# Kernel optimization log

Hardware: AMD Instinct MI355X
Metric: run time of the kernel (lower is better)

## Reference

```python
import jax, jax.numpy as jnp
import numpy as np

HIDDEN = 1024
N_HEADS = 16
HEAD_DIM = HIDDEN // N_HEADS  # 64; RoPE applied only to first HEAD_DIM channels (head 0)
NUM_BUCKETS = 32
MAX_DISTANCE = 128
MLP_HIDDEN = 4 * HIDDEN
B, N = 2, 2048


def _rotate_half(x):
    # interleaved pairs [a0,b0,a1,b1,...] -> [-b0,a0,-b1,a1,...]
    sh = x.shape
    xr = x.reshape(sh[:-1] + (sh[-1] // 2, 2))
    x1, x2 = xr[..., 0], xr[..., 1]
    return jnp.stack([-x2, x1], axis=-1).reshape(sh)


def _rel_bucket(n, num_buckets=NUM_BUCKETS, max_distance=MAX_DISTANCE):
    # bidirectional T5 bucketing
    ctx = jnp.arange(n)[:, None]
    mem = jnp.arange(n)[None, :]
    rp = mem - ctx  # [n, n]
    nb = num_buckets // 2
    buckets = jnp.where(rp > 0, nb, 0)
    rp = jnp.abs(rp)
    max_exact = nb // 2
    is_small = rp < max_exact
    log_ratio = jnp.log(jnp.maximum(rp, 1).astype(jnp.float32) / max_exact)
    rpl = max_exact + (log_ratio / np.log(max_distance / max_exact) * (nb - max_exact)).astype(jnp.int32)
    rpl = jnp.minimum(rpl, nb - 1)
    return buckets + jnp.where(is_small, rp, rpl)


def _ln(x, eps=1e-6):
    # LayerNorm without affine (DiT elementwise_affine=False)
    m = jnp.mean(x, axis=-1, keepdims=True)
    v = jnp.mean(jnp.square(x - m), axis=-1, keepdims=True)
    return (x - m) * jax.lax.rsqrt(v + eps)


def setup_inputs() -> dict:
    key = jax.random.key(0)
    ks = jax.random.split(key, 12)
    s = 0.02
    return {
        "x": jax.random.normal(ks[0], (B, N, HIDDEN), dtype=jnp.float32),
        "c": jax.random.normal(ks[1], (B, HIDDEN), dtype=jnp.float32),
        "w_ada": jax.random.normal(ks[2], (HIDDEN, 6 * HIDDEN), dtype=jnp.float32) * s,
        "b_ada": jnp.zeros((6 * HIDDEN,), dtype=jnp.float32),
        "w_qkv": jax.random.normal(ks[3], (HIDDEN, 3 * HIDDEN), dtype=jnp.float32) * s,
        "b_qkv": jnp.zeros((3 * HIDDEN,), dtype=jnp.float32),
        "w_out": jax.random.normal(ks[4], (HIDDEN, HIDDEN), dtype=jnp.float32) * s,
        "b_out": jnp.zeros((HIDDEN,), dtype=jnp.float32),
        "rel_table": jax.random.normal(ks[5], (NUM_BUCKETS, N_HEADS), dtype=jnp.float32) * s,
        "w_mlp1": jax.random.normal(ks[6], (HIDDEN, MLP_HIDDEN), dtype=jnp.float32) * s,
        "b_mlp1": jnp.zeros((MLP_HIDDEN,), dtype=jnp.float32),
        "w_mlp2": jax.random.normal(ks[7], (MLP_HIDDEN, HIDDEN), dtype=jnp.float32) * s,
        "b_mlp2": jnp.zeros((HIDDEN,), dtype=jnp.float32),
    }


def reference(x, c, w_ada, b_ada, w_qkv, b_qkv, w_out, b_out, rel_table,
              w_mlp1, b_mlp1, w_mlp2, b_mlp2):
    Bb, n, hid = x.shape
    hd = HEAD_DIM

    # AdaLN-Zero modulation params from conditioning
    mod = jax.nn.silu(c) @ w_ada + b_ada  # [B, 6*hid]
    sh_msa, sc_msa, g_msa, sh_mlp, sc_mlp, g_mlp = jnp.split(mod, 6, axis=-1)

    # --- attention branch ---
    h = _ln(x) * (1.0 + sc_msa[:, None, :]) + sh_msa[:, None, :]
    qkv = h @ w_qkv + b_qkv
    q, k, v = jnp.split(qkv, 3, axis=-1)  # each [B, N, hid]

    # partial RoPE: only first head_dim channels (head 0), interleaved-duplicated freqs
    t = jnp.arange(n, dtype=jnp.float32)
    inv_freq = 1.0 / (10000.0 ** (jnp.arange(0, hd, 2, dtype=jnp.float32) / hd))
    fr = t[:, None] * inv_freq[None, :]               # [N, hd/2]
    fr = jnp.stack([fr, fr], axis=-1).reshape(n, hd)  # [N, hd] interleaved dup
    cos, sin = jnp.cos(fr)[None], jnp.sin(fr)[None]

    def partial_rope(a):
        r, u = a[..., :hd], a[..., hd:]
        r = r * cos + _rotate_half(r) * sin
        return jnp.concatenate([r, u], axis=-1)

    q = partial_rope(q)
    k = partial_rope(k)

    qh = q.reshape(Bb, n, N_HEADS, hd)
    kh = k.reshape(Bb, n, N_HEADS, hd)
    vh = v.reshape(Bb, n, N_HEADS, hd)

    scores = jnp.einsum('bqhd,bkhd->bhqk', qh, kh) / np.float32(np.sqrt(hd))
    bias = rel_table[_rel_bucket(n)]                 # [N, N, H]
    scores = scores + jnp.transpose(bias, (2, 0, 1))[None]  # [1,H,N,N]
    attn = jax.nn.softmax(scores, axis=-1)
    ctxv = jnp.einsum('bhqk,bkhd->bqhd', attn, vh).reshape(Bb, n, hid)
    attn_out = ctxv @ w_out + b_out
    x = x + g_msa[:, None, :] * attn_out

    # --- MLP branch ---
    h2 = _ln(x) * (1.0 + sc_mlp[:, None, :]) + sh_mlp[:, None, :]
    m = jax.nn.gelu(h2 @ w_mlp1 + b_mlp1, approximate=True) @ w_mlp2 + b_mlp2
    return x + g_mlp[:, None, :] * m
```

## Files before the change

### kernel.cpp

```cpp
#include <hip/hip_runtime.h>
#include <hip/hip_bf16.h>

#define SEQ 2048

typedef float f32x4 __attribute__((ext_vector_type(4)));
typedef float f32x16 __attribute__((ext_vector_type(16)));
typedef short short8 __attribute__((ext_vector_type(8)));
typedef int int4v __attribute__((ext_vector_type(4)));

static __device__ __forceinline__ unsigned short f2bf(float f) {
  __hip_bfloat16 h = __float2bfloat16(f);
  unsigned short u;
  __builtin_memcpy(&u, &h, 2);
  return u;
}
static __device__ __forceinline__ float bf2f(unsigned short u) {
  __hip_bfloat16 h;
  __builtin_memcpy(&h, &u, 2);
  return __bfloat162float(h);
}
static __device__ __forceinline__ void gload16(const void* g, void* l) {
  __builtin_amdgcn_global_load_lds(
      (const __attribute__((address_space(1))) void*)g,
      (__attribute__((address_space(3))) void*)l, 16, 0, 0);
}
static __device__ __forceinline__ float gelu_t(float x) {
  float t = x * x;
  float z = x * fmaf(0.1029442695044937f, t, 2.3021181827964594f);
  return x * __builtin_amdgcn_rcpf(1.f + exp2f(-z));
}
static __device__ __forceinline__ unsigned int cvtpk(float lo, float hi) {
  unsigned int r;
  asm("v_cvt_pk_bf16_f32 %0, %1, %2" : "=v"(r) : "v"(lo), "v"(hi));
  return r;
}
static __device__ __forceinline__ void rope_pair(short8& v, int m, int i, float pos) {
  const float fr = exp2f(-(float)(2 * i) * (13.287712379549449f / 64.f));
  const float ang = pos * fr;
  const float sn = sinf(ang), cs = cosf(ang);
  const float x0 = bf2f((unsigned short)v[2 * m]);
  const float x1 = bf2f((unsigned short)v[2 * m + 1]);
  v[2 * m] = (short)f2bf(x0 * cs - x1 * sn);
  v[2 * m + 1] = (short)f2bf(x1 * cs + x0 * sn);
}


#define SOFTMAX_M0 16.0f
__global__ void prep_misc(const float* __restrict__ c, float* __restrict__ siluc,
                          const float* __restrict__ rel_table, float* __restrict__ brp) {
  const int bid = blockIdx.x, t = threadIdx.x;
  if (bid < 8) {
    int i = bid * 256 + t;
    float v = c[i];
    siluc[i] = v / (1.f + expf(-v));
  } else {
    int idx = (bid - 8) * 256 + t;
    int h = idx >> 12, pos = idx & 4095;
    int rp = pos - 2047;
    int bucket = rp > 0 ? 16 : 0;
    int a = rp < 0 ? -rp : rp;
    int bi;
    if (a < 8) {
      bi = a;
    } else {
      bi = 8 + (int)(logf((float)a / 8.f) / 2.772588722239781f * 8.f);
      if (bi > 15) bi = 15;
    }
    brp[idx] = rel_table[(bucket + bi) * 16 + h] * 1.4426950408889634f - SOFTMAX_M0;
  }
}

__global__ void mod_part_k(const float* __restrict__ siluc, const float* __restrict__ w_ada,
                           float* __restrict__ part) {
  int gid = blockIdx.x * 256 + threadIdx.x;
  int kc = gid / 12288;
  int idx = gid - kc * 12288;
  int b = idx / 6144;
  int j = idx - b * 6144;
  const float* cp = siluc + b * 1024 + kc * 64;
  const float* wp = w_ada + (size_t)kc * 64 * 6144 + j;
  float acc = 0.f;
#pragma unroll 8
  for (int k = 0; k < 64; ++k) acc += cp[k] * wp[(size_t)k * 6144];
  part[gid] = acc;
}

__global__ void mod_reduce_k(const float* __restrict__ part, const float* __restrict__ b_ada,
                             float* __restrict__ mod) {
  int idx = blockIdx.x * 256 + threadIdx.x;
  int j = idx % 6144;
  float a = b_ada[j];
#pragma unroll
  for (int kc = 0; kc < 16; ++kc) a += part[kc * 12288 + idx];
  mod[idx] = a;
}

__global__ void transpose_all(const float* __restrict__ w_qkv, const float* __restrict__ w_out,
                              const float* __restrict__ w_mlp1, const float* __restrict__ w_mlp2,
                              unsigned short* __restrict__ dq, unsigned short* __restrict__ dwo,
                              unsigned short* __restrict__ dm1, unsigned short* __restrict__ dm2) {
  __shared__ float tile[32][33];
  const int bid = blockIdx.x;
  const float* src;
  unsigned short* dst;
  int K, N, NT, r;
  if (bid < 3072) {
    src = w_qkv; dst = dq; K = 1024; N = 3072; NT = 96; r = bid;
  } else if (bid < 4096) {
    src = w_out; dst = dwo; K = 1024; N = 1024; NT = 32; r = bid - 3072;
  } else if (bid < 8192) {
    src = w_mlp1; dst = dm1; K = 1024; N = 4096; NT = 128; r = bid - 4096;
  } else {
    src = w_mlp2; dst = dm2; K = 4096; N = 1024; NT = 32; r = bid - 8192;
  }
  const int nt = r % NT, kt = r / NT;
  const int t = threadIdx.x;
  const int col = t & 31, r0 = t >> 5;
#pragma unroll
  for (int i = 0; i < 4; ++i) {
    int rr = r0 + i * 8;
    tile[rr][col] = src[(size_t)(kt * 32 + rr) * N + nt * 32 + col];
  }
  __syncthreads();
#pragma unroll
  for (int i = 0; i < 4; ++i) {
    int rr = r0 + i * 8;
    dst[(size_t)(nt * 32 + rr) * K + kt * 32 + col] = f2bf(tile[col][rr]);
  }
}

__global__ void ln_mod(const float* __restrict__ x, const float* __restrict__ mod,
                       unsigned short* __restrict__ out, int sh_off, int sc_off) {
  int row = blockIdx.x;
  int b = row >> 11;
  int t = threadIdx.x;
  const float4 v = ((const float4*)(x + (size_t)row * 1024))[t];
  float s1 = v.x + v.y + v.z + v.w;
  float s2 = v.x * v.x + v.y * v.y + v.z * v.z + v.w * v.w;
#pragma unroll
  for (int off = 32; off; off >>= 1) {
    s1 += __shfl_xor(s1, off);
    s2 += __shfl_xor(s2, off);
  }
  __shared__ float red[8];
  int w = t >> 6, lane = t & 63;
  if (lane == 0) { red[w] = s1; red[4 + w] = s2; }
  __syncthreads();
  s1 = red[0] + red[1] + red[2] + red[3];
  s2 = red[4] + red[5] + red[6] + red[7];
  float mean = s1 * (1.f / 1024.f);
  float var = s2 * (1.f / 1024.f) - mean * mean;
  float rstd = rsqrtf(var + 1e-6f);
  const float* mb = mod + (size_t)b * 6144;
  int col = t * 4;
  ushort4 o4;
  o4.x = f2bf((v.x - mean) * rstd * (1.f + mb[sc_off + col + 0]) + mb[sh_off + col + 0]);
  o4.y = f2bf((v.y - mean) * rstd * (1.f + mb[sc_off + col + 1]) + mb[sh_off + col + 1]);
  o4.z = f2bf((v.z - mean) * rstd * (1.f + mb[sc_off + col + 2]) + mb[sh_off + col + 2]);
  o4.w = f2bf((v.w - mean) * rstd * (1.f + mb[sc_off + col + 3]) + mb[sh_off + col + 3]);
  *((ushort4*)(out + (size_t)row * 1024 + col)) = o4;
}

__global__ void kvpack(const unsigned short* __restrict__ qkv, unsigned short* __restrict__ kpk,
                       unsigned short* __restrict__ vpk) {
  const int kt = blockIdx.x;
  const int bh = blockIdx.y;
  const int b = bh >> 4, h = bh & 15;
  const int t = threadIdx.x;
  const int s = t >> 6, lane = t & 63;
  const int l31 = lane & 31, hi = lane >> 5;
  const size_t outbase = ((size_t)(bh * 64 + kt) * 4 + s) * 512 + lane * 8;
  {
    const unsigned short* src =
        qkv + (size_t)(b * SEQ + kt * 32 + l31) * 3072 + 1024 + h * 64 + s * 16 + hi * 8;
    short8 kv = *(const short8*)src;
    if (h == 0) {
      const float pos = (float)(kt * 32 + l31);
      const int d0 = s * 16 + hi * 8;
#pragma unroll
      for (int m = 0; m < 4; ++m) rope_pair(kv, m, (d0 >> 1) + m, pos);
    }
    *(short8*)(kpk + outbase) = kv;
  }
  {
    const int krow = kt * 32 + (s & 1) * 16 + hi * 8;
    const int d = (s >> 1) * 32 + l31;
    const unsigned short* src = qkv + (size_t)(b * SEQ + krow) * 3072 + 2048 + h * 64 + d;
    unsigned short v[8];
#pragma unroll
    for (int j = 0; j < 8; ++j) v[j] = src[(size_t)j * 3072];
    *(short8*)(vpk + outbase) = *(const short8*)v;
  }
}

template <int MODE, int BM, int BN, int PIPE>
__global__ __launch_bounds__(256) void gemm_bt(
    const unsigned short* __restrict__ A, const unsigned short* __restrict__ Bt,
    const float* __restrict__ bias, void* __restrict__ outp, const float* __restrict__ res,
    const float* __restrict__ mod, int goff, int N, int K) {
  constexpr int NBUF = PIPE ? 2 : 1;
  __shared__ __align__(16) unsigned short a_lds[NBUF][BM * 64];
  __shared__ __align__(16) unsigned short b_lds[NBUF][BN * 64];
  constexpr int WM = BM / 2, WN = BN / 2;
  constexpr int MT = WM / 16, NT = WN / 16;
  const int t = threadIdx.x;
  const int lane = t & 63;
  const int l15 = lane & 15, l4 = lane >> 4;
  const int w = t >> 6;
  const int wr = w >> 1, wc = w & 1;
  const int gx = gridDim.x;
  const int nwg = gx * gridDim.y;
  int wg = blockIdx.y * gx + blockIdx.x;
  wg = (wg & 7) * (nwg >> 3) + (wg >> 3);
  const int by = wg / gx, bx = wg - by * gx;
  const int rowA0 = by * BM;
  const int rowB0 = bx * BN;
  const int wub = t & ~63;

  f32x4 acc[MT][NT];
#pragma unroll
  for (int m = 0; m < MT; ++m)
#pragma unroll
    for (int n = 0; n < NT; ++n) acc[m][n] = (f32x4){0.f, 0.f, 0.f, 0.f};

  auto stage = [&](int buf, int kt) {
#pragma unroll
    for (int rnd = 0; rnd < BM / 32; ++rnd) {
      const int idx = rnd * 256 + t;
      const int row = idx >> 3;
      const int cb = ((idx & 7) << 4) ^ ((row & 7) << 4);
      const char* sa = (const char*)(A + (size_t)(rowA0 + row) * K + kt) + cb;
      gload16(sa, (char*)(&a_lds[buf][0]) + (size_t)(rnd * 256 + wub) * 16);
    }
#pragma unroll
    for (int rnd = 0; rnd < BN / 32; ++rnd) {
      const int idx = rnd * 256 + t;
      const int row = idx >> 3;
      const int cb = ((idx & 7) << 4) ^ ((row & 7) << 4);
      const char* sb = (const char*)(Bt + (size_t)(rowB0 + row) * K + kt) + cb;
      gload16(sb, (char*)(&b_lds[buf][0]) + (size_t)(rnd * 256 + wub) * 16);
    }
  };

  auto compute = [&](int buf) {
#pragma unroll
    for (int kb = 0; kb < 2; ++kb) {
      short8 af[MT], bfr[NT];
#pragma unroll
      for (int m = 0; m < MT; ++m) {
        int row = wr * WM + m * 16 + l15;
        int cb = (kb * 64 + l4 * 16) ^ ((row & 7) << 4);
        af[m] = *(const short8*)((const char*)(&a_lds[buf][0]) + row * 128 + cb);
      }
#pragma unroll
      for (int n = 0; n < NT; ++n) {
        int row = wc * WN + n * 16 + l15;
        int cb = (kb * 64 + l4 * 16) ^ ((row & 7) << 4);
        bfr[n] = *(const short8*)((const char*)(&b_lds[buf][0]) + row * 128 + cb);
      }
      __builtin_amdgcn_s_setprio(1);
#pragma unroll
      for (int m = 0; m < MT; ++m)
#pragma unroll
        for (int n = 0; n < NT; ++n)
          acc[m][n] = __builtin_amdgcn_mfma_f32_16x16x32_bf16(af[m], bfr[n], acc[m][n], 0, 0, 0);
      __builtin_amdgcn_s_setprio(0);
    }
  };

  if (PIPE) {
    stage(0, 0);
    __syncthreads();
    int cur = 0;
    for (int kt = 0; kt < K; kt += 64) {
      if (kt + 64 < K) stage(cur ^ 1, kt + 64);
      compute(cur);
      __syncthreads();
      cur ^= 1;
    }
  } else {
    for (int kt = 0; kt < K; kt += 64) {
      stage(0, kt);
      __syncthreads();
      compute(0);
      __syncthreads();
    }
  }

#pragma unroll
  for (int n = 0; n < NT; ++n) {
    const int col = rowB0 + wc * WN + n * 16 + l15;
    const float bv = bias[col];
#pragma unroll
    for (int m = 0; m < MT; ++m) {
      const int row0 = rowA0 + wr * WM + m * 16 + l4 * 4;
#pragma unroll
      for (int r = 0; r < 4; ++r) {
        float v = acc[m][n][r] + bv;
        const size_t o = (size_t)(row0 + r) * N + col;
        if (MODE == 0) {
          ((unsigned short*)outp)[o] = f2bf(v);
        } else if (MODE == 1) {
          ((unsigned short*)outp)[o] = f2bf(gelu_t(v));
        } else {
          float g = mod[(size_t)((row0 + r) >> 11) * 6144 + goff + col];
          ((float*)outp)[o] = res[o] + g * v;
        }
      }
    }
  }
}

__global__ __launch_bounds__(256) void attn_k(const unsigned short* __restrict__ qkv,
                                              const unsigned short* __restrict__ kpk,
                                              const unsigned short* __restrict__ vpk,
                                              const float* __restrict__ brp_all,
                                              unsigned short* __restrict__ op0,
                                              unsigned short* __restrict__ op1,
                                              float* __restrict__ lpart) {
  const int t = threadIdx.x;
  const int w = t >> 6;
  const int lane = t & 63;
  const int l31 = lane & 31;
  const int hi = lane >> 5;
  const int wg = blockIdx.x;
  const int xcd = wg & 7, idx = wg >> 3;
  const int bh = xcd * 4 + (idx >> 5);
  const int rem = idx & 31;
  const int qt = rem >> 1, ks = rem & 1;
  const int b = bh >> 4, h = bh & 15;
  const int qw = qt * 128 + w * 32;
  const float SC = 0.125f * 1.4426950408889634f;
  const float* brp = brp_all + (size_t)h * 4096;

  short8 qfr[4];
  {
    const unsigned short* qrow = qkv + (size_t)(b * SEQ + qw + l31) * 3072 + h * 64 + hi * 8;
#pragma unroll
    for (int kk = 0; kk < 4; ++kk) qfr[kk] = *(const short8*)(qrow + kk * 16);
    if (h == 0) {
      const float pos = (float)(qw + l31);
#pragma unroll
      for (int kk = 0; kk < 4; ++kk) {
        const int d0 = kk * 16 + hi * 8;
#pragma unroll
        for (int m = 0; m < 4; ++m) rope_pair(qfr[kk], m, (d0 >> 1) + m, pos);
      }
    }
  }
  const float bfar_pos = brp[4095], bfar_neg = brp[0];
  const float* bql = brp + 2047 + 4 * hi - (qw + l31);

  short8 ones;
#pragma unroll
  for (int i = 0; i < 8; ++i) ones[i] = (short)0x3F80;

  const unsigned short* kp = kpk + ((size_t)(bh * 64 + ks * 32)) * 2048 + lane * 8;
  const unsigned short* vp = vpk + ((size_t)(bh * 64 + ks * 32)) * 2048 + lane * 8;

  short8 kfrA[4], vfrA[4], kfrB[4], vfrB[4];
#pragma unroll
  for (int s = 0; s < 4; ++s) {
    kfrA[s] = *(const short8*)(kp + s * 512);
    vfrA[s] = *(const short8*)(vp + s * 512);
  }
  kp += 2048;
  vp += 2048;

  f32x16 oacc0 = {}, oacc1 = {}, lacc = {};
  int kbase = ks * 1024;

#define ATTN_TILE(KF, VF, KFN, VFN)                                                       \
  do {                                                                                    \
    KFN[0] = *(const short8*)(kp);                                                        \
    KFN[1] = *(const short8*)(kp + 512);                                                  \
    KFN[2] = *(const short8*)(kp + 1024);                                                 \
    KFN[3] = *(const short8*)(kp + 1536);                                                 \
    VFN[0] = *(const short8*)(vp);                                                        \
    VFN[1] = *(const short8*)(vp + 512);                                                  \
    VFN[2] = *(const short8*)(vp + 1024);                                                 \
    VFN[3] = *(const short8*)(vp + 1536);                                                 \
    kp += 2048;                                                                           \
    vp += 2048;                                                                           \
    f32x16 sacc = {};                                                                     \
    sacc = __builtin_amdgcn_mfma_f32_32x32x16_bf16(KF[0], qfr[0], sacc, 0, 0, 0);         \
    sacc = __builtin_amdgcn_mfma_f32_32x32x16_bf16(KF[1], qfr[1], sacc, 0, 0, 0);         \
    sacc = __builtin_amdgcn_mfma_f32_32x32x16_bf16(KF[2], qfr[2], sacc, 0, 0, 0);         \
    sacc = __builtin_amdgcn_mfma_f32_32x32x16_bf16(KF[3], qfr[3], sacc, 0, 0, 0);         \
    float p[16];                                                                          \
    const int dd = kbase - qw;                                                            \
    if (dd >= 128 || dd <= -128) {                                                        \
      const float bf_ = (dd > 0) ? bfar_pos : bfar_neg;                                   \
      _Pragma("unroll") for (int r = 0; r < 16; ++r)                                      \
          p[r] = __builtin_amdgcn_exp2f(fmaf(sacc[r], SC, bf_));                          \
    } else {                                                                              \
      const float* bp = bql + kbase;                                                      \
      _Pragma("unroll") for (int r = 0; r < 16; ++r)                                      \
          p[r] = __builtin_amdgcn_exp2f(fmaf(sacc[r], SC, bp[(r & 3) + 8 * (r >> 2)]));   \
    }                                                                                     \
    unsigned int x0 = cvtpk(p[0], p[1]), x1 = cvtpk(p[2], p[3]);                          \
    unsigned int y0 = cvtpk(p[4], p[5]), y1 = cvtpk(p[6], p[7]);                          \
    asm("v_permlane32_swap_b32 %0, %1" : "+v"(x0), "+v"(y0));                             \
    asm("v_permlane32_swap_b32 %0, %1" : "+v"(x1), "+v"(y1));                             \
    unsigned int x2 = cvtpk(p[8], p[9]), x3 = cvtpk(p[10], p[11]);                        \
    unsigned int y2 = cvtpk(p[12], p[13]), y3 = cvtpk(p[14], p[15]);                      \
    asm("v_permlane32_swap_b32 %0, %1" : "+v"(x2), "+v"(y2));                             \
    asm("v_permlane32_swap_b32 %0, %1" : "+v"(x3), "+v"(y3));                             \
    int4v pi0 = {(int)x0, (int)x1, (int)y0, (int)y1};                                     \
    int4v pi1 = {(int)x2, (int)x3, (int)y2, (int)y3};                                     \
    short8 pf0 = __builtin_bit_cast(short8, pi0);                                         \
    short8 pf1 = __builtin_bit_cast(short8, pi1);                                         \
    lacc = __builtin_amdgcn_mfma_f32_32x32x16_bf16(ones, pf0, lacc, 0, 0, 0);             \
    lacc = __builtin_amdgcn_mfma_f32_32x32x16_bf16(ones, pf1, lacc, 0, 0, 0);             \
    oacc0 = __builtin_amdgcn_mfma_f32_32x32x16_bf16(VF[0], pf0, oacc0, 0, 0, 0);          \
    oacc0 = __builtin_amdgcn_mfma_f32_32x32x16_bf16(VF[1], pf1, oacc0, 0, 0, 0);          \
    oacc1 = __builtin_amdgcn_mfma_f32_32x32x16_bf16(VF[2], pf0, oacc1, 0, 0, 0);          \
    oacc1 = __builtin_amdgcn_mfma_f32_32x32x16_bf16(VF[3], pf1, oacc1, 0, 0, 0);          \
    kbase += 32;                                                                          \
  } while (0)

#pragma unroll 1
  for (int it = 0; it < 16; ++it) {
    ATTN_TILE(kfrA, vfrA, kfrB, vfrB);
    ATTN_TILE(kfrB, vfrB, kfrA, vfrA);
  }
#undef ATTN_TILE

  unsigned short* op = ks ? op1 : op0;
  unsigned short* orow = op + (size_t)(b * SEQ + qw + l31) * 1024 + h * 64;
#pragma unroll
  for (int r = 0; r < 16; r += 2) {
    const int d = (r & 3) + 8 * (r >> 2) + 4 * hi;
    *(unsigned int*)(orow + d) = cvtpk(oacc0[r], oacc0[r + 1]);
    *(unsigned int*)(orow + 32 + d) = cvtpk(oacc1[r], oacc1[r + 1]);
  }
  if (lane < 32) lpart[(size_t)ks * 65536 + (size_t)(b * SEQ + qw + l31) * 16 + h] = lacc[0];
}

__global__ void attn_combine(const unsigned short* __restrict__ op0,
                             const unsigned short* __restrict__ op1,
                             const float* __restrict__ lpart,
                             unsigned short* __restrict__ ctxv) {
  const int row = blockIdx.x;
  const int t = threadIdx.x;
  const int h = t >> 4;
  const size_t base = (size_t)row * 1024 + t * 4;
  ushort4 a = *(const ushort4*)(op0 + base);
  ushort4 c = *(const ushort4*)(op1 + base);
  const float l = lpart[(size_t)row * 16 + h] + lpart[65536 + (size_t)row * 16 + h];
  const float inv = 1.f / l;
  ushort4 o;
  o.x = f2bf((bf2f(a.x) + bf2f(c.x)) * inv);
  o.y = f2bf((bf2f(a.y) + bf2f(c.y)) * inv);
  o.z = f2bf((bf2f(a.z) + bf2f(c.z)) * inv);
  o.w = f2bf((bf2f(a.w) + bf2f(c.w)) * inv);
  *(ushort4*)(ctxv + base) = o;
}

extern "C" void kernel_launch(void* const* d_in, const int* in_sizes, int n_in, void* d_out,
                              int out_size, void* d_ws, size_t ws_size, hipStream_t stream) {
  (void)in_sizes; (void)n_in; (void)out_size; (void)ws_size;
  const float* x = (const float*)d_in[0];
  const float* c = (const float*)d_in[1];
  const float* w_ada = (const float*)d_in[2];
  const float* b_ada = (const float*)d_in[3];
  const float* w_qkv = (const float*)d_in[4];
  const float* b_qkv = (const float*)d_in[5];
  const float* w_out = (const float*)d_in[6];
  const float* b_out = (const float*)d_in[7];
  const float* rel_t = (const float*)d_in[8];
  const float* w_mlp1 = (const float*)d_in[9];
  const float* b_mlp1 = (const float*)d_in[10];
  const float* w_mlp2 = (const float*)d_in[11];
  const float* b_mlp2 = (const float*)d_in[12];
  float* out = (float*)d_out;
  char* ws = (char*)d_ws;

  constexpr size_t OFF_WQKVT = 0;
  constexpr size_t OFF_WOUTT = OFF_WQKVT + (size_t)3072 * 1024 * 2;
  constexpr size_t OFF_WM1T = OFF_WOUTT + (size_t)1024 * 1024 * 2;
  constexpr size_t OFF_WM2T = OFF_WM1T + (size_t)4096 * 1024 * 2;
  constexpr size_t OFF_H = OFF_WM2T + (size_t)1024 * 4096 * 2;
  constexpr size_t OFF_QKV = OFF_H + (size_t)4096 * 1024 * 2;
  constexpr size_t OFF_VT = OFF_QKV + (size_t)4096 * 3072 * 2;
  constexpr size_t OFF_CTXV = OFF_VT + (size_t)32 * 64 * 2048 * 2;
  constexpr size_t OFF_MID = OFF_CTXV + (size_t)4096 * 1024 * 2;
  constexpr size_t OFF_SILU = OFF_MID + (size_t)4096 * 4096 * 2;
  constexpr size_t OFF_MOD = OFF_SILU + 2048 * 4;
  constexpr size_t OFF_BRP = OFF_MOD + 12288 * 4;
  constexpr size_t OFF_PART = OFF_BRP + 65536 * 4;
  constexpr size_t OFF_OPART0 = OFF_H;
  constexpr size_t OFF_OPART1 = OFF_MID + (size_t)16 * 1024 * 1024;
  constexpr size_t OFF_LPART = OFF_PART;

  unsigned short* wqkvT = (unsigned short*)(ws + OFF_WQKVT);
  unsigned short* woutT = (unsigned short*)(ws + OFF_WOUTT);
  unsigned short* wm1T = (unsigned short*)(ws + OFF_WM1T);
  unsigned short* wm2T = (unsigned short*)(ws + OFF_WM2T);
  unsigned short* hbuf = (unsigned short*)(ws + OFF_H);
  unsigned short* qkvbuf = (unsigned short*)(ws + OFF_QKV);
  unsigned short* vpkbuf = (unsigned short*)(ws + OFF_VT);
  unsigned short* ctxvbuf = (unsigned short*)(ws + OFF_CTXV);
  unsigned short* midbuf = (unsigned short*)(ws + OFF_MID);
  unsigned short* kpkbuf = (unsigned short*)(ws + OFF_MID);
  float* siluc = (float*)(ws + OFF_SILU);
  float* modb = (float*)(ws + OFF_MOD);
  float* brp = (float*)(ws + OFF_BRP);
  float* part = (float*)(ws + OFF_PART);
  unsigned short* op0 = (unsigned short*)(ws + OFF_OPART0);
  unsigned short* op1 = (unsigned short*)(ws + OFF_OPART1);
  float* lpart = (float*)(ws + OFF_LPART);

  prep_misc<<<264, 256, 0, stream>>>(c, siluc, rel_t, brp);
  mod_part_k<<<768, 256, 0, stream>>>(siluc, w_ada, part);
  mod_reduce_k<<<48, 256, 0, stream>>>(part, b_ada, modb);
  transpose_all<<<12288, 256, 0, stream>>>(w_qkv, w_out, w_mlp1, w_mlp2, wqkvT, woutT, wm1T,
                                           wm2T);

  ln_mod<<<4096, 256, 0, stream>>>(x, modb, hbuf, 0, 1024);
  gemm_bt<0, 128, 128, 0><<<dim3(24, 32), 256, 0, stream>>>(hbuf, wqkvT, b_qkv, qkvbuf, nullptr,
                                                            nullptr, 0, 3072, 1024);
  kvpack<<<dim3(64, 32), 256, 0, stream>>>(qkvbuf, kpkbuf, vpkbuf);
  attn_k<<<1024, 256, 0, stream>>>(qkvbuf, kpkbuf, vpkbuf, brp, op0, op1, lpart);
  attn_combine<<<4096, 256, 0, stream>>>(op0, op1, lpart, ctxvbuf);
  gemm_bt<2, 64, 64, 1><<<dim3(16, 64), 256, 0, stream>>>(ctxvbuf, woutT, b_out, out, x, modb,
                                                          2048, 1024, 1024);
  ln_mod<<<4096, 256, 0, stream>>>(out, modb, hbuf, 3072, 4096);
  gemm_bt<1, 128, 128, 0><<<dim3(32, 32), 256, 0, stream>>>(hbuf, wm1T, b_mlp1, midbuf, nullptr,
                                                            nullptr, 0, 4096, 1024);
  gemm_bt<2, 64, 64, 1><<<dim3(16, 64), 256, 0, stream>>>(midbuf, wm2T, b_mlp2, out, out, modb,
                                                          5120, 1024, 4096);
}
```

Before: 265.6 us.

## Remove split-K in attention and normalize output in-kernel, dropping combine pass

The attention kernel no longer splits the key range across two workgroups. Each workgroup now iterates over all 2048 keys and divides by the row sum before writing bf16 context directly, so the separate combine kernel and its partial-output round trip are removed. In exchange the grid halves to 512 workgroups, each doing twice the serial work, which may reduce occupancy and latency hiding on a 256-CU device.

```diff
diff --git a/kernel.cpp b/kernel.cpp
--- a/kernel.cpp
+++ b/kernel.cpp
@@ -315,9 +315,7 @@
                                               const unsigned short* __restrict__ kpk,
                                               const unsigned short* __restrict__ vpk,
                                               const float* __restrict__ brp_all,
-                                              unsigned short* __restrict__ op0,
-                                              unsigned short* __restrict__ op1,
-                                              float* __restrict__ lpart) {
+                                              unsigned short* __restrict__ ctxv) {
   const int t = threadIdx.x;
   const int w = t >> 6;
   const int lane = t & 63;
@@ -325,9 +323,8 @@
   const int hi = lane >> 5;
   const int wg = blockIdx.x;
   const int xcd = wg & 7, idx = wg >> 3;
-  const int bh = xcd * 4 + (idx >> 5);
-  const int rem = idx & 31;
-  const int qt = rem >> 1, ks = rem & 1;
+  const int bh = xcd * 4 + (idx >> 4);
+  const int qt = idx & 15;
   const int b = bh >> 4, h = bh & 15;
   const int qw = qt * 128 + w * 32;
   const float SC = 0.125f * 1.4426950408889634f;
@@ -355,8 +352,8 @@
 #pragma unroll
   for (int i = 0; i < 8; ++i) ones[i] = (short)0x3F80;
 
-  const unsigned short* kp = kpk + ((size_t)(bh * 64 + ks * 32)) * 2048 + lane * 8;
-  const unsigned short* vp = vpk + ((size_t)(bh * 64 + ks * 32)) * 2048 + lane * 8;
+  const unsigned short* kp = kpk + ((size_t)(bh * 64)) * 2048 + lane * 8;
+  const unsigned short* vp = vpk + ((size_t)(bh * 64)) * 2048 + lane * 8;
 
   short8 kfrA[4], vfrA[4], kfrB[4], vfrB[4];
 #pragma unroll
@@ -368,7 +365,7 @@
   vp += 2048;
 
   f32x16 oacc0 = {}, oacc1 = {}, lacc = {};
-  int kbase = ks * 1024;
+  int kbase = 0;
 
 #define ATTN_TILE(KF, VF, KFN, VFN)                                                       \
   do {                                                                                    \
@@ -420,41 +417,20 @@
   } while (0)
 
 #pragma unroll 1
-  for (int it = 0; it < 16; ++it) {
+  for (int it = 0; it < 32; ++it) {
     ATTN_TILE(kfrA, vfrA, kfrB, vfrB);
     ATTN_TILE(kfrB, vfrB, kfrA, vfrA);
   }
 #undef ATTN_TILE
 
-  unsigned short* op = ks ? op1 : op0;
-  unsigned short* orow = op + (size_t)(b * SEQ + qw + l31) * 1024 + h * 64;
+  const float inv = 1.f / lacc[0];
+  unsigned short* orow = ctxv + (size_t)(b * SEQ + qw + l31) * 1024 + h * 64;
 #pragma unroll
   for (int r = 0; r < 16; r += 2) {
     const int d = (r & 3) + 8 * (r >> 2) + 4 * hi;
-    *(unsigned int*)(orow + d) = cvtpk(oacc0[r], oacc0[r + 1]);
-    *(unsigned int*)(orow + 32 + d) = cvtpk(oacc1[r], oacc1[r + 1]);
-  }
-  if (lane < 32) lpart[(size_t)ks * 65536 + (size_t)(b * SEQ + qw + l31) * 16 + h] = lacc[0];
-}
-
-__global__ void attn_combine(const unsigned short* __restrict__ op0,
-                             const unsigned short* __restrict__ op1,
-                             const float* __restrict__ lpart,
-                             unsigned short* __restrict__ ctxv) {
-  const int row = blockIdx.x;
-  const int t = threadIdx.x;
-  const int h = t >> 4;
-  const size_t base = (size_t)row * 1024 + t * 4;
-  ushort4 a = *(const ushort4*)(op0 + base);
-  ushort4 c = *(const ushort4*)(op1 + base);
-  const float l = lpart[(size_t)row * 16 + h] + lpart[65536 + (size_t)row * 16 + h];
-  const float inv = 1.f / l;
-  ushort4 o;
-  o.x = f2bf((bf2f(a.x) + bf2f(c.x)) * inv);
-  o.y = f2bf((bf2f(a.y) + bf2f(c.y)) * inv);
-  o.z = f2bf((bf2f(a.z) + bf2f(c.z)) * inv);
-  o.w = f2bf((bf2f(a.w) + bf2f(c.w)) * inv);
-  *(ushort4*)(ctxv + base) = o;
+    *(unsigned int*)(orow + d) = cvtpk(oacc0[r] * inv, oacc0[r + 1] * inv);
+    *(unsigned int*)(orow + 32 + d) = cvtpk(oacc1[r] * inv, oacc1[r + 1] * inv);
+  }
 }
 
 extern "C" void kernel_launch(void* const* d_in, const int* in_sizes, int n_in, void* d_out,
@@ -489,9 +465,6 @@
   constexpr size_t OFF_MOD = OFF_SILU + 2048 * 4;
   constexpr size_t OFF_BRP = OFF_MOD + 12288 * 4;
   constexpr size_t OFF_PART = OFF_BRP + 65536 * 4;
-  constexpr size_t OFF_OPART0 = OFF_H;
-  constexpr size_t OFF_OPART1 = OFF_MID + (size_t)16 * 1024 * 1024;
-  constexpr size_t OFF_LPART = OFF_PART;
 
   unsigned short* wqkvT = (unsigned short*)(ws + OFF_WQKVT);
   unsigned short* woutT = (unsigned short*)(ws + OFF_WOUTT);
@@ -507,9 +480,6 @@
   float* modb = (float*)(ws + OFF_MOD);
   float* brp = (float*)(ws + OFF_BRP);
   float* part = (float*)(ws + OFF_PART);
-  unsigned short* op0 = (unsigned short*)(ws + OFF_OPART0);
-  unsigned short* op1 = (unsigned short*)(ws + OFF_OPART1);
-  float* lpart = (float*)(ws + OFF_LPART);
 
   prep_misc<<<264, 256, 0, stream>>>(c, siluc, rel_t, brp);
   mod_part_k<<<768, 256, 0, stream>>>(siluc, w_ada, part);
@@ -521,8 +491,7 @@
   gemm_bt<0, 128, 128, 0><<<dim3(24, 32), 256, 0, stream>>>(hbuf, wqkvT, b_qkv, qkvbuf, nullptr,
                                                             nullptr, 0, 3072, 1024);
   kvpack<<<dim3(64, 32), 256, 0, stream>>>(qkvbuf, kpkbuf, vpkbuf);
-  attn_k<<<1024, 256, 0, stream>>>(qkvbuf, kpkbuf, vpkbuf, brp, op0, op1, lpart);
-  attn_combine<<<4096, 256, 0, stream>>>(op0, op1, lpart, ctxvbuf);
+  attn_k<<<512, 256, 0, stream>>>(qkvbuf, kpkbuf, vpkbuf, brp, ctxvbuf);
   gemm_bt<2, 64, 64, 1><<<dim3(16, 64), 256, 0, stream>>>(ctxvbuf, woutT, b_out, out, x, modb,
                                                           2048, 1024, 1024);
   ln_mod<<<4096, 256, 0, stream>>>(out, modb, hbuf, 3072, 4096);
```

Result: faster. 255.5 us (-3.8%).
